# Kernel optimization log

Measured on AMD Instinct MI355X. Metric: run time of the kernel, lower is better.

## Reference

```python
import jax, jax.numpy as jnp
import numpy as np

HIDDEN_DIM = 2048
NUM_HEADS = 16
HEAD_DIM = HIDDEN_DIM // NUM_HEADS


def setup_inputs() -> dict:
    key = jax.random.key(0)
    ks = jax.random.split(key, 5)
    B, S, D = 1, 2048, HIDDEN_DIM
    scale = 1.0 / np.sqrt(D)
    return {
        "x": jax.random.normal(ks[0], (B, S, D), dtype=jnp.float32),
        "w_q": jax.random.normal(ks[1], (D, D), dtype=jnp.float32) * scale,
        "w_k": jax.random.normal(ks[2], (D, D), dtype=jnp.float32) * scale,
        "w_v": jax.random.normal(ks[3], (D, D), dtype=jnp.float32) * scale,
        "w_o": jax.random.normal(ks[4], (D, D), dtype=jnp.float32) * scale,
    }


def reference(x, w_q, w_k, w_v, w_o):
    # x: (B, S, D). Projections use x @ W.T as in the torch module.
    B, S, D = x.shape
    H, Hd = NUM_HEADS, HEAD_DIM
    q = (x @ w_q.T).reshape(B, S, H, Hd)
    k = (x @ w_k.T).reshape(B, S, H, Hd)
    v = (x @ w_v.T).reshape(B, S, H, Hd)
    scale = 1.0 / np.sqrt(Hd).astype(np.float32)
    # The tiled online-softmax loop computes exact softmax attention.
    scores = jnp.einsum("bqhd,bkhd->bhqk", q, k) * scale  # (B,H,S,S)
    p = jax.nn.softmax(scores, axis=-1)
    o = jnp.einsum("bhqk,bkhd->bqhd", p, v).reshape(B, S, D)
    return o @ w_o.T
```

## Files before the change

kernel.cpp:

```cpp
#include <hip/hip_runtime.h>
#include <hip/hip_bf16.h>
#include <cstdint>
#include <cstddef>

typedef __bf16 bf16x8 __attribute__((ext_vector_type(8)));
typedef float f32x4 __attribute__((ext_vector_type(4)));
typedef unsigned short u16x8 __attribute__((ext_vector_type(8)));
typedef unsigned short u16x4 __attribute__((ext_vector_type(4)));

#define S_LEN 2048
#define DMODEL 2048
#define NHEADS 16
#define HD 128

__device__ inline unsigned short f2bf(float f) {
  union { float f; unsigned int u; } v; v.f = f;
  unsigned int r = (v.u + 0x7fffu + ((v.u >> 16) & 1u)) >> 16;
  return (unsigned short)r;
}

__device__ __forceinline__ void gload16(const unsigned short* g,
                                        unsigned short* lds) {
  __builtin_amdgcn_global_load_lds(
      (const __attribute__((address_space(1))) void*)g,
      (__attribute__((address_space(3))) void*)lds, 16, 0, 0);
}

__global__ void cast_all(const float* __restrict__ x, const float* __restrict__ wq,
                         const float* __restrict__ wk, const float* __restrict__ wv,
                         const float* __restrict__ wo,
                         unsigned short* __restrict__ out, float qscale) {
  const int b = blockIdx.x;
  const int seg = b >> 12;
  const int i = ((b & 4095) * 256 + threadIdx.x) * 4;
  const float* src = seg == 0 ? x : seg == 1 ? wq : seg == 2 ? wk
                   : seg == 3 ? wv : wo;
  const float scale = (seg == 1) ? qscale : 1.0f;
  unsigned short* dst = out + (size_t)seg * ((size_t)S_LEN * DMODEL);
  float4 v = *(const float4*)(src + i);
  u16x4 o;
  o.x = f2bf(v.x * scale); o.y = f2bf(v.y * scale);
  o.z = f2bf(v.z * scale); o.w = f2bf(v.w * scale);
  *(u16x4*)(dst + i) = o;
}

template <int MODE>
__device__ __forceinline__ void gemm_core(
    const unsigned short* __restrict__ A, const unsigned short* __restrict__ B,
    unsigned short* __restrict__ Cb,
    int M, int N, int K, int m0, int n0,
    unsigned short* As, unsigned short* Bs) {
  constexpr int BK = 32;
  const int tid = threadIdx.x;
  const int wave = tid >> 6, lane = tid & 63;
  const int lg = lane >> 4, lr = lane & 15;
  const int rw = (wave >> 1) * 64;
  const int cw = (wave & 1) * 64;

  const int c0 = tid, c1 = tid + 256;
  const unsigned short* Ap0 = A + (size_t)(m0 + (c0 >> 2)) * K + (c0 & 3) * 8;
  const unsigned short* Ap1 = A + (size_t)(m0 + (c1 >> 2)) * K + (c1 & 3) * 8;
  const unsigned short* Bp0 = B + (size_t)(n0 + (c0 >> 2)) * K + (c0 & 3) * 8;
  const unsigned short* Bp1 = B + (size_t)(n0 + (c1 >> 2)) * K + (c1 & 3) * 8;
  unsigned short* as0 = As + wave * 512;
  unsigned short* as1 = As + 2048 + wave * 512;
  unsigned short* bs0 = Bs + wave * 512;
  unsigned short* bs1 = Bs + 2048 + wave * 512;

  f32x4 acc[4][4];
#pragma unroll
  for (int i = 0; i < 4; i++)
#pragma unroll
    for (int j = 0; j < 4; j++) acc[i][j] = (f32x4){0.f, 0.f, 0.f, 0.f};

  const int nk = K / BK;
  for (int kt = 0; kt < nk; ++kt) {
    const int ko = kt * BK;
    __syncthreads();
    gload16(Ap0 + ko, as0);
    gload16(Ap1 + ko, as1);
    gload16(Bp0 + ko, bs0);
    gload16(Bp1 + ko, bs1);
    __syncthreads();

    bf16x8 af[4], bfr[4];
#pragma unroll
    for (int mt = 0; mt < 4; mt++)
      af[mt] = *(const bf16x8*)(As + (rw + mt * 16 + lr) * BK + lg * 8);
#pragma unroll
    for (int nt = 0; nt < 4; nt++)
      bfr[nt] = *(const bf16x8*)(Bs + (cw + nt * 16 + lr) * BK + lg * 8);
#pragma unroll
    for (int mt = 0; mt < 4; mt++)
#pragma unroll
      for (int nt = 0; nt < 4; nt++)
        acc[mt][nt] = __builtin_amdgcn_mfma_f32_16x16x32_bf16(
            af[mt], bfr[nt], acc[mt][nt], 0, 0, 0);
  }

#pragma unroll
  for (int mt = 0; mt < 4; mt++)
#pragma unroll
    for (int nt = 0; nt < 4; nt++) {
      const int col = n0 + cw + nt * 16 + lr;
#pragma unroll
      for (int r = 0; r < 4; r++) {
        const int row = m0 + rw + mt * 16 + lg * 4 + r;
        const float v = acc[mt][nt][r];
        if (MODE == 1) Cb[(size_t)row * N + col] = f2bf(v);
        else Cb[(size_t)col * M + row] = f2bf(v);
      }
    }
}

__global__ __launch_bounds__(256, 2) void gemm_qkv(
    const unsigned short* __restrict__ xb, const unsigned short* __restrict__ wqb,
    const unsigned short* __restrict__ wkb, const unsigned short* __restrict__ wvb,
    unsigned short* __restrict__ qb, unsigned short* __restrict__ kb,
    unsigned short* __restrict__ vTb) {
  __shared__ unsigned short As[128 * 32];
  __shared__ unsigned short Bs[128 * 32];
  const int which = blockIdx.x >> 4;
  const int n0 = (blockIdx.x & 15) * 128;
  const int m0 = blockIdx.y * 128;
  if (which == 0)
    gemm_core<1>(xb, wqb, qb, S_LEN, DMODEL, DMODEL, m0, n0, As, Bs);
  else if (which == 1)
    gemm_core<1>(xb, wkb, kb, S_LEN, DMODEL, DMODEL, m0, n0, As, Bs);
  else
    gemm_core<2>(xb, wvb, vTb, S_LEN, DMODEL, DMODEL, m0, n0, As, Bs);
}

__global__ __launch_bounds__(256, 2) void gemm_bt64(
    const unsigned short* __restrict__ A, const unsigned short* __restrict__ B,
    float* __restrict__ Cf, int M, int N, int K) {
  constexpr int BK = 32;
  __shared__ unsigned short As[64 * 32];
  __shared__ unsigned short Bs[128 * 32];
  const int tid = threadIdx.x;
  const int wave = tid >> 6, lane = tid & 63;
  const int lg = lane >> 4, lr = lane & 15;
  const int rw = (wave >> 1) * 32;
  const int cw = (wave & 1) * 64;
  const int m0 = blockIdx.y * 64, n0 = blockIdx.x * 128;

  const int c0 = tid, c1 = tid + 256;
  const unsigned short* Ap0 = A + (size_t)(m0 + (c0 >> 2)) * K + (c0 & 3) * 8;
  const unsigned short* Bp0 = B + (size_t)(n0 + (c0 >> 2)) * K + (c0 & 3) * 8;
  const unsigned short* Bp1 = B + (size_t)(n0 + (c1 >> 2)) * K + (c1 & 3) * 8;
  unsigned short* as0 = As + wave * 512;
  unsigned short* bs0 = Bs + wave * 512;
  unsigned short* bs1 = Bs + 2048 + wave * 512;

  f32x4 acc[2][4];
#pragma unroll
  for (int i = 0; i < 2; i++)
#pragma unroll
    for (int j = 0; j < 4; j++) acc[i][j] = (f32x4){0.f, 0.f, 0.f, 0.f};

  const int nk = K / BK;
  for (int kt = 0; kt < nk; ++kt) {
    const int ko = kt * BK;
    __syncthreads();
    gload16(Ap0 + ko, as0);
    gload16(Bp0 + ko, bs0);
    gload16(Bp1 + ko, bs1);
    __syncthreads();

    bf16x8 af[2], bfr[4];
#pragma unroll
    for (int mt = 0; mt < 2; mt++)
      af[mt] = *(const bf16x8*)(As + (rw + mt * 16 + lr) * BK + lg * 8);
#pragma unroll
    for (int nt = 0; nt < 4; nt++)
      bfr[nt] = *(const bf16x8*)(Bs + (cw + nt * 16 + lr) * BK + lg * 8);
#pragma unroll
    for (int mt = 0; mt < 2; mt++)
#pragma unroll
      for (int nt = 0; nt < 4; nt++)
        acc[mt][nt] = __builtin_amdgcn_mfma_f32_16x16x32_bf16(
            af[mt], bfr[nt], acc[mt][nt], 0, 0, 0);
  }

#pragma unroll
  for (int mt = 0; mt < 2; mt++)
#pragma unroll
    for (int nt = 0; nt < 4; nt++) {
      const int col = n0 + cw + nt * 16 + lr;
#pragma unroll
      for (int r = 0; r < 4; r++) {
        const int row = m0 + rw + mt * 16 + lg * 4 + r;
        Cf[(size_t)row * N + col] = acc[mt][nt][r];
      }
    }
}

__global__ __launch_bounds__(256, 2) void attn_kernel(
    const unsigned short* __restrict__ q, const unsigned short* __restrict__ k,
    const unsigned short* __restrict__ vT, unsigned short* __restrict__ o) {
  constexpr int KT = 64;
  constexpr int KSP = KT + 8;
  __shared__ unsigned short Ks[KT * 136];
  __shared__ unsigned short Vt[HD * KSP];
  __shared__ unsigned short Ps[64 * 64];

  const int tid = threadIdx.x;
  const int w = tid >> 6, lane = tid & 63;
  const int lg = lane >> 4, lr = lane & 15;
  const int h = blockIdx.y;
  const int q0 = blockIdx.x * 64;
  const int qw = q0 + w * 16;

  bf16x8 qf[4];
#pragma unroll
  for (int ks = 0; ks < 4; ks++)
    qf[ks] = *(const bf16x8*)(q + (size_t)(qw + lr) * DMODEL + h * HD +
                              ks * 32 + lg * 8);

  f32x4 Oacc[8];
#pragma unroll
  for (int j = 0; j < 8; j++) Oacc[j] = (f32x4){0.f, 0.f, 0.f, 0.f};
  float lst[4] = {0.f, 0.f, 0.f, 0.f};

  int krow[4], kcg[4], vrow[4], vcg[4];
#pragma unroll
  for (int i = 0; i < 4; i++) {
    const int c = i * 256 + tid;
    krow[i] = c >> 4; kcg[i] = c & 15;
    vrow[i] = c >> 3; vcg[i] = c & 7;
  }

  u16x8 kreg[4], vreg[4];
#pragma unroll
  for (int i = 0; i < 4; i++) {
    kreg[i] = *(const u16x8*)(k + (size_t)(krow[i]) * DMODEL + h * HD + kcg[i] * 8);
    vreg[i] = *(const u16x8*)(vT + (size_t)(h * HD + vrow[i]) * S_LEN + vcg[i] * 8);
  }

  for (int kt = 0; kt < S_LEN / KT; ++kt) {
    __syncthreads();
#pragma unroll
    for (int i = 0; i < 4; i++) {
      *(u16x8*)(Ks + krow[i] * 136 + kcg[i] * 8) = kreg[i];
      *(u16x8*)(Vt + vrow[i] * KSP + vcg[i] * 8) = vreg[i];
    }
    __syncthreads();

    if (kt + 1 < S_LEN / KT) {
      const int kbase = (kt + 1) * KT;
#pragma unroll
      for (int i = 0; i < 4; i++) {
        kreg[i] = *(const u16x8*)(k + (size_t)(kbase + krow[i]) * DMODEL +
                                  h * HD + kcg[i] * 8);
        vreg[i] = *(const u16x8*)(vT + (size_t)(h * HD + vrow[i]) * S_LEN +
                                  kbase + vcg[i] * 8);
      }
    }

    f32x4 sc[4];
#pragma unroll
    for (int j = 0; j < 4; j++) sc[j] = (f32x4){0.f, 0.f, 0.f, 0.f};
#pragma unroll
    for (int ks = 0; ks < 4; ks++) {
      bf16x8 kf[4];
#pragma unroll
      for (int nt = 0; nt < 4; nt++)
        kf[nt] = *(const bf16x8*)(Ks + (nt * 16 + lr) * 136 + ks * 32 + lg * 8);
#pragma unroll
      for (int nt = 0; nt < 4; nt++)
        sc[nt] = __builtin_amdgcn_mfma_f32_16x16x32_bf16(qf[ks], kf[nt],
                                                         sc[nt], 0, 0, 0);
    }

#pragma unroll
    for (int r = 0; r < 4; r++) {
      const int rowbase = (w * 16 + lg * 4 + r) * 64;
#pragma unroll
      for (int nt = 0; nt < 4; nt++) {
        const float p = __builtin_amdgcn_exp2f(sc[nt][r]);
        lst[r] += p;
        union { float f; unsigned int u; } cv; cv.f = p;
        Ps[rowbase + ((nt * 16 + lr + lg * 16) & 63)] =
            (unsigned short)(cv.u >> 16);
      }
    }

    const int lrot = ((lr >> 2) & 3) * 16;
#pragma unroll
    for (int ks = 0; ks < 2; ks++) {
      const bf16x8 pf = *(const bf16x8*)(
          Ps + (w * 16 + lr) * 64 + ((ks * 32 + lg * 8 + lrot) & 63));
#pragma unroll
      for (int nt = 0; nt < 8; nt++) {
        const bf16x8 vf =
            *(const bf16x8*)(Vt + (nt * 16 + lr) * KSP + ks * 32 + lg * 8);
        Oacc[nt] = __builtin_amdgcn_mfma_f32_16x16x32_bf16(pf, vf, Oacc[nt],
                                                           0, 0, 0);
      }
    }
  }

#pragma unroll
  for (int r = 0; r < 4; r++) {
    float rs = lst[r];
    rs += __shfl_xor(rs, 1);
    rs += __shfl_xor(rs, 2);
    rs += __shfl_xor(rs, 4);
    rs += __shfl_xor(rs, 8);
    const float inv = 1.0f / rs;
    const int row = qw + lg * 4 + r;
#pragma unroll
    for (int nt = 0; nt < 8; nt++)
      o[(size_t)row * DMODEL + h * HD + nt * 16 + lr] =
          f2bf(Oacc[nt][r] * inv);
  }
}

extern "C" void kernel_launch(void* const* d_in, const int* in_sizes, int n_in,
                              void* d_out, int out_size, void* d_ws, size_t ws_size,
                              hipStream_t stream) {
  (void)in_sizes; (void)n_in; (void)out_size; (void)ws_size;
  const float* x  = (const float*)d_in[0];
  const float* wq = (const float*)d_in[1];
  const float* wk = (const float*)d_in[2];
  const float* wv = (const float*)d_in[3];
  const float* wo = (const float*)d_in[4];
  float* out = (float*)d_out;

  const size_t NE = (size_t)S_LEN * DMODEL;
  unsigned short* ws = (unsigned short*)d_ws;
  unsigned short* xb  = ws + 0 * NE;
  unsigned short* wqb = ws + 1 * NE;
  unsigned short* wkb = ws + 2 * NE;
  unsigned short* wvb = ws + 3 * NE;
  unsigned short* wob = ws + 4 * NE;
  unsigned short* qb  = ws + 5 * NE;
  unsigned short* kb  = ws + 6 * NE;
  unsigned short* vTb = ws + 7 * NE;
  unsigned short* ob  = ws + 8 * NE;

  const float qscale = 0.08838834764831845f * 1.4426950408889634f;

  cast_all<<<dim3(5 * 4096), dim3(256), 0, stream>>>(x, wq, wk, wv, wo, ws,
                                                     qscale);

  gemm_qkv<<<dim3(48, 16), dim3(256), 0, stream>>>(xb, wqb, wkb, wvb, qb, kb,
                                                   vTb);

  attn_kernel<<<dim3(S_LEN / 64, NHEADS), dim3(256), 0, stream>>>(qb, kb, vTb,
                                                                  ob);

  gemm_bt64<<<dim3(16, 32), dim3(256), 0, stream>>>(ob, wob, out, S_LEN,
                                                    DMODEL, DMODEL);
}
```

Baseline: 271.2 us.

## Restructure attention kernel to 32x32x16 MFMA with 2x2 wave split

```diff
diff --git a/kernel.cpp b/kernel.cpp
--- a/kernel.cpp
+++ b/kernel.cpp
@@ -5,6 +5,7 @@
 
 typedef __bf16 bf16x8 __attribute__((ext_vector_type(8)));
 typedef float f32x4 __attribute__((ext_vector_type(4)));
+typedef float f32x16 __attribute__((ext_vector_type(16)));
 typedef unsigned short u16x8 __attribute__((ext_vector_type(8)));
 typedef unsigned short u16x4 __attribute__((ext_vector_type(4)));
 
@@ -199,28 +200,31 @@
     const unsigned short* __restrict__ q, const unsigned short* __restrict__ k,
     const unsigned short* __restrict__ vT, unsigned short* __restrict__ o) {
   constexpr int KT = 64;
-  constexpr int KSP = KT + 8;
-  __shared__ unsigned short Ks[KT * 136];
-  __shared__ unsigned short Vt[HD * KSP];
-  __shared__ unsigned short Ps[64 * 64];
+  __shared__ unsigned short Ks[64 * 136];
+  __shared__ unsigned short Vt[128 * 72];
+  __shared__ unsigned short Ps[64 * 72];
+  __shared__ float Lred[4][32];
 
   const int tid = threadIdx.x;
   const int w = tid >> 6, lane = tid & 63;
-  const int lg = lane >> 4, lr = lane & 15;
+  const int l32 = lane & 31, lh = lane >> 5;
+  const int qh = w >> 1;
+  const int kh = w & 1;
   const int h = blockIdx.y;
   const int q0 = blockIdx.x * 64;
-  const int qw = q0 + w * 16;
-
-  bf16x8 qf[4];
-#pragma unroll
-  for (int ks = 0; ks < 4; ks++)
-    qf[ks] = *(const bf16x8*)(q + (size_t)(qw + lr) * DMODEL + h * HD +
-                              ks * 32 + lg * 8);
-
-  f32x4 Oacc[8];
-#pragma unroll
-  for (int j = 0; j < 8; j++) Oacc[j] = (f32x4){0.f, 0.f, 0.f, 0.f};
-  float lst[4] = {0.f, 0.f, 0.f, 0.f};
+
+  bf16x8 qf[8];
+#pragma unroll
+  for (int ks = 0; ks < 8; ks++)
+    qf[ks] = *(const bf16x8*)(q + (size_t)(q0 + qh * 32 + l32) * DMODEL +
+                              h * HD + ks * 16 + lh * 8);
+
+  f32x16 Oacc[2];
+#pragma unroll
+  for (int mt = 0; mt < 2; mt++)
+#pragma unroll
+    for (int j = 0; j < 16; j++) Oacc[mt][j] = 0.f;
+  float lsum = 0.f;
 
   int krow[4], kcg[4], vrow[4], vcg[4];
 #pragma unroll
@@ -229,7 +233,6 @@
     krow[i] = c >> 4; kcg[i] = c & 15;
     vrow[i] = c >> 3; vcg[i] = c & 7;
   }
-
   u16x8 kreg[4], vreg[4];
 #pragma unroll
   for (int i = 0; i < 4; i++) {
@@ -237,16 +240,17 @@
     vreg[i] = *(const u16x8*)(vT + (size_t)(h * HD + vrow[i]) * S_LEN + vcg[i] * 8);
   }
 
-  for (int kt = 0; kt < S_LEN / KT; ++kt) {
+  constexpr int NT = S_LEN / KT;
+  for (int kt = 0; kt < NT; ++kt) {
     __syncthreads();
 #pragma unroll
     for (int i = 0; i < 4; i++) {
       *(u16x8*)(Ks + krow[i] * 136 + kcg[i] * 8) = kreg[i];
-      *(u16x8*)(Vt + vrow[i] * KSP + vcg[i] * 8) = vreg[i];
-    }
-    __syncthreads();
-
-    if (kt + 1 < S_LEN / KT) {
+      *(u16x8*)(Vt + vrow[i] * 72 + vcg[i] * 8) = vreg[i];
+    }
+    __syncthreads();
+
+    if (kt + 1 < NT) {
       const int kbase = (kt + 1) * KT;
 #pragma unroll
       for (int i = 0; i < 4; i++) {
@@ -257,62 +261,68 @@
       }
     }
 
-    f32x4 sc[4];
-#pragma unroll
-    for (int j = 0; j < 4; j++) sc[j] = (f32x4){0.f, 0.f, 0.f, 0.f};
-#pragma unroll
-    for (int ks = 0; ks < 4; ks++) {
-      bf16x8 kf[4];
-#pragma unroll
-      for (int nt = 0; nt < 4; nt++)
-        kf[nt] = *(const bf16x8*)(Ks + (nt * 16 + lr) * 136 + ks * 32 + lg * 8);
-#pragma unroll
-      for (int nt = 0; nt < 4; nt++)
-        sc[nt] = __builtin_amdgcn_mfma_f32_16x16x32_bf16(qf[ks], kf[nt],
-                                                         sc[nt], 0, 0, 0);
-    }
-
-#pragma unroll
-    for (int r = 0; r < 4; r++) {
-      const int rowbase = (w * 16 + lg * 4 + r) * 64;
-#pragma unroll
-      for (int nt = 0; nt < 4; nt++) {
-        const float p = __builtin_amdgcn_exp2f(sc[nt][r]);
-        lst[r] += p;
+    f32x16 sacc;
+#pragma unroll
+    for (int j = 0; j < 16; j++) sacc[j] = 0.f;
+#pragma unroll
+    for (int ks = 0; ks < 8; ks++) {
+      const bf16x8 kf =
+          *(const bf16x8*)(Ks + (kh * 32 + l32) * 136 + ks * 16 + lh * 8);
+      sacc = __builtin_amdgcn_mfma_f32_32x32x16_bf16(kf, qf[ks], sacc, 0, 0, 0);
+    }
+
+#pragma unroll
+    for (int rq = 0; rq < 4; rq++) {
+      u16x4 pk;
+#pragma unroll
+      for (int ri = 0; ri < 4; ri++) {
+        const float p = __builtin_amdgcn_exp2f(sacc[rq * 4 + ri]);
+        lsum += p;
         union { float f; unsigned int u; } cv; cv.f = p;
-        Ps[rowbase + ((nt * 16 + lr + lg * 16) & 63)] =
-            (unsigned short)(cv.u >> 16);
-      }
-    }
-
-    const int lrot = ((lr >> 2) & 3) * 16;
-#pragma unroll
-    for (int ks = 0; ks < 2; ks++) {
-      const bf16x8 pf = *(const bf16x8*)(
-          Ps + (w * 16 + lr) * 64 + ((ks * 32 + lg * 8 + lrot) & 63));
-#pragma unroll
-      for (int nt = 0; nt < 8; nt++) {
-        const bf16x8 vf =
-            *(const bf16x8*)(Vt + (nt * 16 + lr) * KSP + ks * 32 + lg * 8);
-        Oacc[nt] = __builtin_amdgcn_mfma_f32_16x16x32_bf16(pf, vf, Oacc[nt],
-                                                           0, 0, 0);
-      }
-    }
-  }
-
-#pragma unroll
-  for (int r = 0; r < 4; r++) {
-    float rs = lst[r];
-    rs += __shfl_xor(rs, 1);
-    rs += __shfl_xor(rs, 2);
-    rs += __shfl_xor(rs, 4);
-    rs += __shfl_xor(rs, 8);
-    const float inv = 1.0f / rs;
-    const int row = qw + lg * 4 + r;
-#pragma unroll
-    for (int nt = 0; nt < 8; nt++)
-      o[(size_t)row * DMODEL + h * HD + nt * 16 + lr] =
-          f2bf(Oacc[nt][r] * inv);
+        pk[ri] = (unsigned short)(cv.u >> 16);
+      }
+      *(u16x4*)(Ps + (qh * 32 + l32) * 72 + kh * 32 + rq * 8 + lh * 4) = pk;
+    }
+    __syncthreads();
+
+#pragma unroll
+    for (int ks2 = 0; ks2 < 4; ks2++) {
+      const bf16x8 pfr =
+          *(const bf16x8*)(Ps + (qh * 32 + l32) * 72 + ks2 * 16 + lh * 8);
+#pragma unroll
+      for (int mt = 0; mt < 2; mt++) {
+        const bf16x8 vf = *(const bf16x8*)(
+            Vt + (kh * 64 + mt * 32 + l32) * 72 + ks2 * 16 + lh * 8);
+        Oacc[mt] =
+            __builtin_amdgcn_mfma_f32_32x32x16_bf16(vf, pfr, Oacc[mt], 0, 0, 0);
+      }
+    }
+  }
+
+  lsum += __shfl_xor(lsum, 32);
+  if (lh == 0) Lred[w][l32] = lsum;
+  __syncthreads();
+  const float ltot = Lred[qh * 2][l32] + Lred[qh * 2 + 1][l32];
+  const float inv = 1.0f / ltot;
+
+#pragma unroll
+  for (int mt = 0; mt < 2; mt++)
+#pragma unroll
+    for (int rq = 0; rq < 4; rq++) {
+      u16x4 pk;
+#pragma unroll
+      for (int ri = 0; ri < 4; ri++)
+        pk[ri] = f2bf(Oacc[mt][rq * 4 + ri] * inv);
+      *(u16x4*)(Ks + (qh * 32 + l32) * 136 + kh * 64 + mt * 32 + rq * 8 +
+                lh * 4) = pk;
+    }
+  __syncthreads();
+#pragma unroll
+  for (int i = 0; i < 4; i++) {
+    const int c = i * 256 + tid;
+    const int row = c >> 4, ch = c & 15;
+    const u16x8 vv = *(const u16x8*)(Ks + row * 136 + ch * 8);
+    *(u16x8*)(o + (size_t)(q0 + row) * DMODEL + h * HD + ch * 8) = vv;
   }
 }
 
```

After: 258.2 us. 1.05x faster.
